# Performance work log

Hardware: AMD Instinct MI355X
Metric: run time of the kernel (lower is better)

The kernel has to match this reference:

```python
import jax, jax.numpy as jnp
import numpy as np

K = 3
EPS = 1e-08
N_SRC = 65536   # source points
M_QRY = 262144  # query points
C_FEAT = 128


def setup_inputs() -> dict:
    key = jax.random.key(0)
    k1, k2, k3, k4 = jax.random.split(key, 4)
    s_feats = jax.random.normal(k1, (N_SRC, C_FEAT), dtype=jnp.float32)
    q_points = jax.random.normal(k2, (M_QRY, 3), dtype=jnp.float32)
    s_points = jax.random.normal(k3, (N_SRC, 3), dtype=jnp.float32)
    neighbor_indices = jax.random.randint(k4, (M_QRY, K), 0, N_SRC, dtype=jnp.int64)
    return {
        "s_feats": s_feats,
        "q_points": q_points,
        "s_points": s_points,
        "neighbor_indices": neighbor_indices,
    }


def reference(s_feats, q_points, s_points, neighbor_indices):
    # k-NN inverse-distance interpolation (k > 1 branch of KNNInterpolate)
    knn_idx = neighbor_indices[:, :K]            # [M, k]
    knn_points = s_points[knn_idx]               # [M, k, 3] gather
    knn_feats = s_feats[knn_idx]                 # [M, k, C] gather
    # squared distances query -> each neighbor
    d2 = jnp.sum((q_points[:, None, :] - knn_points) ** 2, axis=-1)  # [M, k]
    w = 1.0 / (d2 + EPS)                          # inverse-distance weights
    w = w / jnp.sum(w, axis=-1, keepdims=True)    # normalize over k
    q_feats = jnp.einsum("mk,mkc->mc", w, knn_feats)  # weighted reduction
    return q_feats
```

## Files before the change

### kernel.cpp

```cpp
#include <hip/hip_runtime.h>

#define KNN_EPS 1e-8f
#define C_FEAT 128
#define M_QRY 262144
#define QPT 4

typedef float f4 __attribute__((ext_vector_type(4)));

__global__ __launch_bounds__(256) void knn_interp_kernel(
    const float* __restrict__ s_feats,
    const float* __restrict__ q_points,
    const float* __restrict__ s_points,
    const int*   __restrict__ nbr_idx,
    float* __restrict__ out)
{
    const int t  = blockIdx.x * blockDim.x + threadIdx.x;
    const int g  = t >> 5;
    const int c4 = t & 31;
    const int mbase = g * QPT;

    int idx[QPT][3];
#pragma unroll
    for (int q = 0; q < QPT; ++q) {
#pragma unroll
        for (int k = 0; k < 3; ++k)
            idx[q][k] = nbr_idx[(mbase + q) * 3 + k];
    }

    f4 v[QPT][3];
#pragma unroll
    for (int q = 0; q < QPT; ++q) {
#pragma unroll
        for (int k = 0; k < 3; ++k)
            v[q][k] = ((const f4*)(s_feats + (size_t)idx[q][k] * C_FEAT))[c4];
    }

    float w[QPT][3];
#pragma unroll
    for (int q = 0; q < QPT; ++q) {
        const int m = mbase + q;
        const float qx = q_points[m * 3 + 0];
        const float qy = q_points[m * 3 + 1];
        const float qz = q_points[m * 3 + 2];
#pragma unroll
        for (int k = 0; k < 3; ++k) {
            const int s = idx[q][k];
            const float dx = qx - s_points[s * 3 + 0];
            const float dy = qy - s_points[s * 3 + 1];
            const float dz = qz - s_points[s * 3 + 2];
            w[q][k] = __builtin_amdgcn_rcpf(dx * dx + dy * dy + dz * dz + KNN_EPS);
        }
    }

#pragma unroll
    for (int q = 0; q < QPT; ++q) {
        const float inv = __builtin_amdgcn_rcpf(w[q][0] + w[q][1] + w[q][2]);
        const f4 r = (w[q][0] * inv) * v[q][0]
                   + (w[q][1] * inv) * v[q][1]
                   + (w[q][2] * inv) * v[q][2];
        __builtin_nontemporal_store(r, (f4*)(out + (size_t)(mbase + q) * C_FEAT) + c4);
    }
}

extern "C" void kernel_launch(void* const* d_in, const int* in_sizes, int n_in,
                              void* d_out, int out_size, void* d_ws, size_t ws_size,
                              hipStream_t stream) {
    const float* s_feats  = (const float*)d_in[0];
    const float* q_points = (const float*)d_in[1];
    const float* s_points = (const float*)d_in[2];
    const int*   nbr_idx  = (const int*)d_in[3];
    float* out = (float*)d_out;

    const int total_threads = M_QRY * 32 / QPT;
    const int block = 256;
    const int grid  = (total_threads + block - 1) / block;

    knn_interp_kernel<<<grid, block, 0, stream>>>(s_feats, q_points, s_points,
                                                  nbr_idx, out);
}
```

Measured before the change: 208.4 us.

## Convert source features to fp16 in a pre-pass and gather half-precision rows

```diff
diff --git a/kernel.cpp b/kernel.cpp
--- a/kernel.cpp
+++ b/kernel.cpp
@@ -2,13 +2,24 @@
 
 #define KNN_EPS 1e-8f
 #define C_FEAT 128
+#define N_SRC 65536
 #define M_QRY 262144
-#define QPT 4
+#define QPT 2
 
 typedef float f4 __attribute__((ext_vector_type(4)));
+typedef _Float16 h4 __attribute__((ext_vector_type(4)));
+
+__global__ __launch_bounds__(256) void cvt_feats_kernel(
+    const float* __restrict__ s_feats, _Float16* __restrict__ ws)
+{
+    const int t = blockIdx.x * blockDim.x + threadIdx.x;
+    const f4 a = ((const f4*)s_feats)[t];
+    const h4 h = __builtin_convertvector(a, h4);
+    __builtin_nontemporal_store(h, (h4*)ws + t);
+}
 
 __global__ __launch_bounds__(256) void knn_interp_kernel(
-    const float* __restrict__ s_feats,
+    const _Float16* __restrict__ feats16,
     const float* __restrict__ q_points,
     const float* __restrict__ s_points,
     const int*   __restrict__ nbr_idx,
@@ -21,19 +32,17 @@
 
     int idx[QPT][3];
 #pragma unroll
-    for (int q = 0; q < QPT; ++q) {
+    for (int q = 0; q < QPT; ++q)
 #pragma unroll
         for (int k = 0; k < 3; ++k)
             idx[q][k] = nbr_idx[(mbase + q) * 3 + k];
-    }
 
-    f4 v[QPT][3];
+    h4 v[QPT][3];
 #pragma unroll
-    for (int q = 0; q < QPT; ++q) {
+    for (int q = 0; q < QPT; ++q)
 #pragma unroll
         for (int k = 0; k < 3; ++k)
-            v[q][k] = ((const f4*)(s_feats + (size_t)idx[q][k] * C_FEAT))[c4];
-    }
+            v[q][k] = ((const h4*)(feats16 + (size_t)idx[q][k] * C_FEAT))[c4];
 
     float w[QPT][3];
 #pragma unroll
@@ -55,9 +64,9 @@
 #pragma unroll
     for (int q = 0; q < QPT; ++q) {
         const float inv = __builtin_amdgcn_rcpf(w[q][0] + w[q][1] + w[q][2]);
-        const f4 r = (w[q][0] * inv) * v[q][0]
-                   + (w[q][1] * inv) * v[q][1]
-                   + (w[q][2] * inv) * v[q][2];
+        const f4 r = (w[q][0] * inv) * __builtin_convertvector(v[q][0], f4)
+                   + (w[q][1] * inv) * __builtin_convertvector(v[q][1], f4)
+                   + (w[q][2] * inv) * __builtin_convertvector(v[q][2], f4);
         __builtin_nontemporal_store(r, (f4*)(out + (size_t)(mbase + q) * C_FEAT) + c4);
     }
 }
@@ -70,11 +79,17 @@
     const float* s_points = (const float*)d_in[2];
     const int*   nbr_idx  = (const int*)d_in[3];
     float* out = (float*)d_out;
+    _Float16* feats16 = (_Float16*)d_ws;
 
-    const int total_threads = M_QRY * 32 / QPT;
-    const int block = 256;
-    const int grid  = (total_threads + block - 1) / block;
+    {
+        const int total = N_SRC * C_FEAT / 4;
+        cvt_feats_kernel<<<total / 256, 256, 0, stream>>>(s_feats, feats16);
+    }
 
-    knn_interp_kernel<<<grid, block, 0, stream>>>(s_feats, q_points, s_points,
-                                                  nbr_idx, out);
+    {
+        const int total_threads = M_QRY * 32 / QPT;
+        const int grid = total_threads / 256;
+        knn_interp_kernel<<<grid, 256, 0, stream>>>(feats16, q_points, s_points,
+                                                    nbr_idx, out);
+    }
 }
```

Result: no change. 204.4 us (-1.9%).
